# Kernel optimization log

Measured on AMD Instinct MI355X. Metric: run time of the kernel, lower is better.

## Reference

```python
import jax, jax.numpy as jnp
import numpy as np

N_NODES = 100000
N_EDGES = 3200000
F_IN = 54
H = 16


def gcn_conv(x, edge_index, W, b):
    """PyG GCNConv: linear -> add self-loops -> sym-normalized scatter-add -> +bias."""
    n = x.shape[0]
    x = x @ W  # [N, H] transform before propagation (PyG order)
    loop = jnp.arange(n, dtype=edge_index.dtype)
    src = jnp.concatenate([edge_index[0], loop])  # message sources
    dst = jnp.concatenate([edge_index[1], loop])  # aggregation targets
    deg = jax.ops.segment_sum(jnp.ones_like(dst, dtype=x.dtype), dst, num_segments=n)
    dinv = jnp.where(deg > 0, jax.lax.rsqrt(deg), 0.0)
    norm = dinv[src] * dinv[dst]  # D^-1/2 A_hat D^-1/2 edge weights
    msg = x[src] * norm[:, None]  # gather + scale, [E+N, H]
    out = jax.ops.segment_sum(msg, dst, num_segments=n)  # scatter-add
    return out + b


def setup_inputs() -> dict:
    key = jax.random.key(0)
    k = jax.random.split(key, 6)
    x = jax.random.normal(k[0], (N_NODES, F_IN), dtype=jnp.float32)
    edge_index = jax.random.randint(k[1], (2, N_EDGES), 0, N_NODES, dtype=jnp.int64)
    # Glorot-style init for GCNConv weights; bias zeros (PyG default)
    s1 = float(np.sqrt(6.0 / (F_IN + H)))
    s2 = float(np.sqrt(6.0 / (H + H)))
    W1 = jax.random.uniform(k[2], (F_IN, H), dtype=jnp.float32, minval=-s1, maxval=s1)
    b1 = jnp.zeros((H,), dtype=jnp.float32)
    W2 = jax.random.uniform(k[3], (H, H), dtype=jnp.float32, minval=-s2, maxval=s2)
    b2 = jnp.zeros((H,), dtype=jnp.float32)
    return {"x": x, "edge_index": edge_index, "W1": W1, "b1": b1, "W2": W2, "b2": b2}


def reference(x, edge_index, W1, b1, W2, b2):
    h = jax.nn.relu(gcn_conv(x, edge_index, W1, b1))
    # F.dropout(p=0.5, training=self.training) -> identity in eval mode
    h = jax.nn.relu(gcn_conv(h, edge_index, W2, b2))
    return h
```

## Files before the change

### kernel.cpp

```cpp
#include <hip/hip_runtime.h>
#include <hip/hip_fp16.h>

#define HDIM 16
#define FIN 54
#define BSHIFT 7
#define BNODES (1 << BSHIFT)
#define NBMAXB 800
#define NBBMAX 512
#define FBT 1024
#define LST 512
#define FPE 12544
#define PADCOL 6144
#define GTILE 256
#define GPAD 55

__global__ __launch_bounds__(FBT)
void fill_binned_kernel(const int* __restrict__ src, const int* __restrict__ dst,
                        int* __restrict__ lps, unsigned int* __restrict__ binned,
                        int E, int nb, int nbb, int per) {
    __shared__ unsigned int stage[FPE];
    __shared__ int lh[NBMAXB], lcur[NBMAXB];
    __shared__ int ls[FBT];
    int blk = blockIdx.x;
    int s0 = blk * per;
    int s1 = min(E, s0 + per);
    int tot = s1 - s0;
    int t = threadIdx.x;

    for (int b = t; b < nb; b += FBT) lh[b] = 0;
    __syncthreads();
    int idx = s0 + (t << 2);
    for (; idx + 3 < s1; idx += (FBT << 2)) {
        int4 d4 = *(const int4*)&dst[idx];
        atomicAdd(&lh[d4.x >> BSHIFT], 1);
        atomicAdd(&lh[d4.y >> BSHIFT], 1);
        atomicAdd(&lh[d4.z >> BSHIFT], 1);
        atomicAdd(&lh[d4.w >> BSHIFT], 1);
    }
    if (idx < s1) {
        int stop = min(idx + 4, s1);
        for (int e = idx; e < stop; ++e) atomicAdd(&lh[dst[e] >> BSHIFT], 1);
    }
    __syncthreads();
    ls[t] = (t < nb) ? lh[t] : 0;
    __syncthreads();
    for (int d = 1; d < FBT; d <<= 1) {
        int v = (t >= d) ? ls[t - d] : 0;
        __syncthreads();
        ls[t] += v;
        __syncthreads();
    }
    if (t <= nb) {
        int excl = ls[t] - ((t < nb) ? lh[t] : 0);
        if (t < nb) lcur[t] = excl;
        lps[t * nbb + blk] = excl;
    }
    __syncthreads();
    idx = s0 + (t << 2);
    for (; idx + 3 < s1; idx += (FBT << 2)) {
        int4 d4 = *(const int4*)&dst[idx];
        int4 v4 = *(const int4*)&src[idx];
        int p0 = atomicAdd(&lcur[d4.x >> BSHIFT], 1);
        int p1 = atomicAdd(&lcur[d4.y >> BSHIFT], 1);
        int p2 = atomicAdd(&lcur[d4.z >> BSHIFT], 1);
        int p3 = atomicAdd(&lcur[d4.w >> BSHIFT], 1);
        stage[p0] = ((unsigned int)v4.x << BSHIFT) | (unsigned int)(d4.x & (BNODES - 1));
        stage[p1] = ((unsigned int)v4.y << BSHIFT) | (unsigned int)(d4.y & (BNODES - 1));
        stage[p2] = ((unsigned int)v4.z << BSHIFT) | (unsigned int)(d4.z & (BNODES - 1));
        stage[p3] = ((unsigned int)v4.w << BSHIFT) | (unsigned int)(d4.w & (BNODES - 1));
    }
    if (idx < s1) {
        int stop = min(idx + 4, s1);
        for (int e = idx; e < stop; ++e) {
            int d = dst[e];
            int pos = atomicAdd(&lcur[d >> BSHIFT], 1);
            stage[pos] = ((unsigned int)src[e] << BSHIFT) | (unsigned int)(d & (BNODES - 1));
        }
    }
    __syncthreads();
    for (int k = t; k < tot; k += FBT) binned[s0 + k] = stage[k];
}

__global__ __launch_bounds__(LST)
void local_sort_kernel(const unsigned int* __restrict__ binned,
                       const int* __restrict__ lps,
                       unsigned int* __restrict__ col, int* __restrict__ cs,
                       int* __restrict__ ce, float* __restrict__ dinv,
                       int n, int nb, int nbb, int per) {
    __shared__ int st[NBBMAX], en[NBBMAX];
    __shared__ int hist[BNODES], scn[BNODES], cur[BNODES];
    int b = blockIdx.x;
    int t = threadIdx.x;
    int colbase = b * PADCOL;

    for (int blk = t; blk < nbb; blk += LST) {
        st[blk] = lps[b * nbb + blk];
        en[blk] = lps[(b + 1) * nbb + blk];
    }
    if (t < BNODES) hist[t] = 0;
    __syncthreads();

    int g = t >> 4, l = t & 15;
    for (int blk = g; blk < nbb; blk += (LST >> 4)) {
        int base = blk * per;
        int e = en[blk];
        for (int k = st[blk] + l; k < e; k += 16)
            atomicAdd(&hist[binned[base + k] & (BNODES - 1)], 1);
    }
    __syncthreads();
    if (t < BNODES) scn[t] = hist[t];
    __syncthreads();
    for (int d = 1; d < BNODES; d <<= 1) {
        int v = (t < BNODES && t >= d) ? scn[t - d] : 0;
        __syncthreads();
        if (t < BNODES) scn[t] += v;
        __syncthreads();
    }
    if (t < BNODES) {
        int excl = scn[t] - hist[t];
        cur[t] = excl;
        int node = (b << BSHIFT) + t;
        if (node < n) {
            cs[node] = colbase + excl;
            ce[node] = colbase + excl + hist[t];
            dinv[node] = rsqrtf((float)hist[t] + 1.0f);
        }
    }
    __syncthreads();
    for (int blk = g; blk < nbb; blk += (LST >> 4)) {
        int base = blk * per;
        int e = en[blk];
        for (int k = st[blk] + l; k < e; k += 16) {
            unsigned int p = binned[base + k];
            int pos = atomicAdd(&cur[p & (BNODES - 1)], 1);
            col[colbase + pos] = p >> BSHIFT;
        }
    }
}

__global__ __launch_bounds__(256)
void gemm_kernel(const float* __restrict__ X, const float* __restrict__ W,
                 const float* __restrict__ dinv, __half* __restrict__ Yh, int n) {
    __shared__ float Wl[FIN * HDIM];
    __shared__ float xl[GTILE * GPAD];
    for (int t = threadIdx.x; t < FIN * HDIM; t += blockDim.x) Wl[t] = W[t];

    int base = blockIdx.x * GTILE;
    int nrows = min(GTILE, n - base);
    const float* xb = X + (size_t)base * FIN;
    int tot = nrows * FIN;
    for (int i4 = threadIdx.x; i4 < (tot >> 2); i4 += blockDim.x) {
        float4 v = ((const float4*)xb)[i4];
        int i = i4 << 2;
        int r = i / FIN;
        int c = i - r * FIN;
#pragma unroll
        for (int u = 0; u < 4; ++u) {
            int cc = c + u, rr = r;
            if (cc >= FIN) { cc -= FIN; ++rr; }
            xl[rr * GPAD + cc] = (&v.x)[u];
        }
    }
    for (int i = (tot & ~3) + threadIdx.x; i < tot; i += blockDim.x) {
        int r = i / FIN;
        xl[r * GPAD + (i - r * FIN)] = xb[i];
    }
    __syncthreads();

    int t = threadIdx.x;
    if (t < nrows) {
        int row = base + t;
        const float* xr = &xl[t * GPAD];
        float acc[HDIM];
#pragma unroll
        for (int j = 0; j < HDIM; ++j) acc[j] = 0.0f;
#pragma unroll
        for (int k = 0; k < FIN; ++k) {
            float xv = xr[k];
#pragma unroll
            for (int j = 0; j < HDIM; ++j)
                acc[j] = fmaf(xv, Wl[k * HDIM + j], acc[j]);
        }
        float di = dinv[row];
        __half2 hh[8];
#pragma unroll
        for (int j = 0; j < 8; ++j)
            hh[j] = __floats2half2_rn(di * acc[2 * j], di * acc[2 * j + 1]);
        uint4* yo = (uint4*)(Yh + ((size_t)row << 4));
        yo[0] = *(uint4*)&hh[0];
        yo[1] = *(uint4*)&hh[4];
    }
}

__device__ __forceinline__ float4 ld_h4(const __half* __restrict__ hsh,
                                        unsigned int node, int q) {
    uint2 u = *(const uint2*)(hsh + ((size_t)node << 4) + (q << 2));
    __half2 a = *(__half2*)&u.x;
    __half2 b = *(__half2*)&u.y;
    float2 fa = __half22float2(a);
    float2 fb = __half22float2(b);
    return make_float4(fa.x, fa.y, fb.x, fb.y);
}

template <bool FUSE_W2>
__global__ void gather_kernel(const unsigned int* __restrict__ col,
                              const int* __restrict__ cs, const int* __restrict__ ce,
                              const __half* __restrict__ hsh, const float* __restrict__ dinv,
                              const float* __restrict__ bias, const float* __restrict__ W2,
                              __half* __restrict__ outh, float4* __restrict__ out4, int n) {
    __shared__ float4 W2l[HDIM * 4];
    if constexpr (FUSE_W2) {
        for (int t = threadIdx.x; t < HDIM * 4; t += blockDim.x)
            W2l[t] = ((const float4*)W2)[t];
        __syncthreads();
    }
    int idx = blockIdx.x * blockDim.x + threadIdx.x;
    int i = idx >> 3;
    int sub = idx & 7;
    int q = sub & 3;
    int h = sub >> 2;
    if (i >= n) return;
    int k0 = cs[i], k1 = ce[i];

    float4 acc = (h == 0) ? ld_h4(hsh, (unsigned int)i, q)
                          : make_float4(0.f, 0.f, 0.f, 0.f);
    int k = k0 + h;
    for (; k + 14 < k1; k += 16) {
        unsigned int s[8];
#pragma unroll
        for (int u = 0; u < 8; ++u) s[u] = col[k + 2 * u];
        float4 hv[8];
#pragma unroll
        for (int u = 0; u < 8; ++u) hv[u] = ld_h4(hsh, s[u], q);
#pragma unroll
        for (int u = 0; u < 8; ++u) {
            acc.x += hv[u].x; acc.y += hv[u].y; acc.z += hv[u].z; acc.w += hv[u].w;
        }
    }
    for (; k < k1; k += 2) {
        float4 hv = ld_h4(hsh, col[k], q);
        acc.x += hv.x; acc.y += hv.y; acc.z += hv.z; acc.w += hv.w;
    }
    acc.x += __shfl_xor(acc.x, 4);
    acc.y += __shfl_xor(acc.y, 4);
    acc.z += __shfl_xor(acc.z, 4);
    acc.w += __shfl_xor(acc.w, 4);

    float di = dinv[i];
    float4 b4 = ((const float4*)bias)[q];
    float4 r;
    r.x = fmaxf(fmaf(di, acc.x, b4.x), 0.0f);
    r.y = fmaxf(fmaf(di, acc.y, b4.y), 0.0f);
    r.z = fmaxf(fmaf(di, acc.z, b4.z), 0.0f);
    r.w = fmaxf(fmaf(di, acc.w, b4.w), 0.0f);

    if constexpr (FUSE_W2) {
        int lane = threadIdx.x & 63;
        int base = lane & ~7;
        float4 o = make_float4(0.f, 0.f, 0.f, 0.f);
#pragma unroll
        for (int p = 0; p < 4; ++p) {
            float rx = __shfl(r.x, base + p, 64);
            float ry = __shfl(r.y, base + p, 64);
            float rz = __shfl(r.z, base + p, 64);
            float rw = __shfl(r.w, base + p, 64);
            float4 w0 = W2l[(p * 4 + 0) * 4 + q];
            float4 w1 = W2l[(p * 4 + 1) * 4 + q];
            float4 w2 = W2l[(p * 4 + 2) * 4 + q];
            float4 w3 = W2l[(p * 4 + 3) * 4 + q];
            o.x = fmaf(rx, w0.x, fmaf(ry, w1.x, fmaf(rz, w2.x, fmaf(rw, w3.x, o.x))));
            o.y = fmaf(rx, w0.y, fmaf(ry, w1.y, fmaf(rz, w2.y, fmaf(rw, w3.y, o.y))));
            o.z = fmaf(rx, w0.z, fmaf(ry, w1.z, fmaf(rz, w2.z, fmaf(rw, w3.z, o.z))));
            o.w = fmaf(rx, w0.w, fmaf(ry, w1.w, fmaf(rz, w2.w, fmaf(rw, w3.w, o.w))));
        }
        if (h == 0) {
            __half2 o01 = __floats2half2_rn(di * o.x, di * o.y);
            __half2 o23 = __floats2half2_rn(di * o.z, di * o.w);
            uint2 pk;
            pk.x = *(unsigned int*)&o01;
            pk.y = *(unsigned int*)&o23;
            *(uint2*)(outh + ((size_t)i << 4) + (q << 2)) = pk;
        }
    } else {
        if (h == 0) out4[(size_t)i * 4 + q] = r;
    }
}

extern "C" void kernel_launch(void* const* d_in, const int* in_sizes, int n_in,
                              void* d_out, int out_size, void* d_ws, size_t ws_size,
                              hipStream_t stream) {
    const float* x  = (const float*)d_in[0];
    const int*   ei = (const int*)d_in[1];
    const float* W1 = (const float*)d_in[2];
    const float* b1 = (const float*)d_in[3];
    const float* W2 = (const float*)d_in[4];
    const float* b2 = (const float*)d_in[5];
    float* out = (float*)d_out;

    const int E = in_sizes[1] / 2;
    const int n = in_sizes[0] / FIN;
    const int* src = ei;
    const int* dst = ei + E;
    const int nb = (n + BNODES - 1) >> BSHIFT;

    int nbb = (E + 12499) / 12500;
    if (nbb > NBBMAX) nbb = NBBMAX;
    int per = (((E + nbb - 1) / nbb) + 3) & ~3;

    char* w = (char*)d_ws;
    auto take = [&](size_t bytes) { char* p = w; w += (bytes + 255) & ~(size_t)255; return p; };
    float* dinv = (float*)take((size_t)n * 4);
    int*   lps  = (int*)take((size_t)(nb + 1) * nbb * 4);
    int*   cs   = (int*)take((size_t)n * 4);
    int*   ce   = (int*)take((size_t)n * 4);
    size_t binned_sz = (size_t)nbb * per * 4;
    size_t h_sz      = (size_t)n * HDIM * 2 * 2;
    char*  X    = take(binned_sz > h_sz ? binned_sz : h_sz);
    unsigned int* binned = (unsigned int*)X;
    __half* hA  = (__half*)X;
    __half* hB  = (__half*)(X + (size_t)n * HDIM * 2);
    unsigned int* col = (unsigned int*)take((size_t)nb * PADCOL * 4);

    const int B = 256;

    fill_binned_kernel<<<nbb, FBT, 0, stream>>>(src, dst, lps, binned, E, nb, nbb, per);
    local_sort_kernel<<<nb, LST, 0, stream>>>(binned, lps, col, cs, ce, dinv, n, nb, nbb, per);

    gemm_kernel<<<(n + GTILE - 1) / GTILE, B, 0, stream>>>(x, W1, dinv, hA, n);

    gather_kernel<true><<<(n * 8 + B - 1) / B, B, 0, stream>>>(
        col, cs, ce, hA, dinv, b1, W2, hB, nullptr, n);

    gather_kernel<false><<<(n * 8 + B - 1) / B, B, 0, stream>>>(
        col, cs, ce, hB, dinv, b2, nullptr, nullptr, (float4*)out, n);
}
```

Baseline: 109.7 us.

## Fuse first-layer GEMM into the local sort kernel per node block

The separate X@W1 GEMM kernel is merged into the per-128-node local sort kernel. Each block loads its 128 rows of x and W1 into shared memory, computes the transformed features after the sort, and scales them by the degree normalisation it just computed in registers. This removes one kernel launch and the dinv reload. The cost is higher shared-memory use and only 128 of the 512 threads doing the GEMM. The binned and hA buffers no longer alias, since both are now live at the same time.

Result: faster. 102.3 us (-6.7%).

```diff
diff --git a/kernel.cpp b/kernel.cpp
--- a/kernel.cpp
+++ b/kernel.cpp
@@ -11,7 +11,6 @@
 #define LST 512
 #define FPE 12544
 #define PADCOL 6144
-#define GTILE 256
 #define GPAD 55
 
 __global__ __launch_bounds__(FBT)
@@ -82,16 +81,42 @@
 }
 
 __global__ __launch_bounds__(LST)
-void local_sort_kernel(const unsigned int* __restrict__ binned,
-                       const int* __restrict__ lps,
-                       unsigned int* __restrict__ col, int* __restrict__ cs,
-                       int* __restrict__ ce, float* __restrict__ dinv,
-                       int n, int nb, int nbb, int per) {
+void sort_gemm_kernel(const unsigned int* __restrict__ binned,
+                      const int* __restrict__ lps,
+                      const float* __restrict__ x, const float* __restrict__ W1,
+                      unsigned int* __restrict__ col, int* __restrict__ cs,
+                      int* __restrict__ ce, float* __restrict__ dinv,
+                      __half* __restrict__ hA,
+                      int n, int nb, int nbb, int per) {
     __shared__ int st[NBBMAX], en[NBBMAX];
     __shared__ int hist[BNODES], scn[BNODES], cur[BNODES];
+    __shared__ float Wl[FIN * HDIM];
+    __shared__ float xl[BNODES * GPAD];
     int b = blockIdx.x;
     int t = threadIdx.x;
     int colbase = b * PADCOL;
+    int row0 = b << BSHIFT;
+    int nrows = min(BNODES, n - row0);
+
+    const float* xb = x + (size_t)row0 * FIN;
+    int tot = nrows * FIN;
+    for (int i4 = t; i4 < (tot >> 2); i4 += LST) {
+        float4 v = ((const float4*)xb)[i4];
+        int i = i4 << 2;
+        int r = i / FIN;
+        int c = i - r * FIN;
+#pragma unroll
+        for (int u = 0; u < 4; ++u) {
+            int cc = c + u, rr = r;
+            if (cc >= FIN) { cc -= FIN; ++rr; }
+            xl[rr * GPAD + cc] = (&v.x)[u];
+        }
+    }
+    for (int i = (tot & ~3) + t; i < tot; i += LST) {
+        int r = i / FIN;
+        xl[r * GPAD + (i - r * FIN)] = xb[i];
+    }
+    for (int k = t; k < FIN * HDIM; k += LST) Wl[k] = W1[k];
 
     for (int blk = t; blk < nbb; blk += LST) {
         st[blk] = lps[b * nbb + blk];
@@ -116,14 +141,16 @@
         if (t < BNODES) scn[t] += v;
         __syncthreads();
     }
+    float di = 0.0f;
     if (t < BNODES) {
         int excl = scn[t] - hist[t];
         cur[t] = excl;
-        int node = (b << BSHIFT) + t;
+        int node = row0 + t;
+        di = rsqrtf((float)hist[t] + 1.0f);
         if (node < n) {
             cs[node] = colbase + excl;
             ce[node] = colbase + excl + hist[t];
-            dinv[node] = rsqrtf((float)hist[t] + 1.0f);
+            dinv[node] = di;
         }
     }
     __syncthreads();
@@ -136,40 +163,7 @@
             col[colbase + pos] = p >> BSHIFT;
         }
     }
-}
-
-__global__ __launch_bounds__(256)
-void gemm_kernel(const float* __restrict__ X, const float* __restrict__ W,
-                 const float* __restrict__ dinv, __half* __restrict__ Yh, int n) {
-    __shared__ float Wl[FIN * HDIM];
-    __shared__ float xl[GTILE * GPAD];
-    for (int t = threadIdx.x; t < FIN * HDIM; t += blockDim.x) Wl[t] = W[t];
-
-    int base = blockIdx.x * GTILE;
-    int nrows = min(GTILE, n - base);
-    const float* xb = X + (size_t)base * FIN;
-    int tot = nrows * FIN;
-    for (int i4 = threadIdx.x; i4 < (tot >> 2); i4 += blockDim.x) {
-        float4 v = ((const float4*)xb)[i4];
-        int i = i4 << 2;
-        int r = i / FIN;
-        int c = i - r * FIN;
-#pragma unroll
-        for (int u = 0; u < 4; ++u) {
-            int cc = c + u, rr = r;
-            if (cc >= FIN) { cc -= FIN; ++rr; }
-            xl[rr * GPAD + cc] = (&v.x)[u];
-        }
-    }
-    for (int i = (tot & ~3) + threadIdx.x; i < tot; i += blockDim.x) {
-        int r = i / FIN;
-        xl[r * GPAD + (i - r * FIN)] = xb[i];
-    }
-    __syncthreads();
-
-    int t = threadIdx.x;
     if (t < nrows) {
-        int row = base + t;
         const float* xr = &xl[t * GPAD];
         float acc[HDIM];
 #pragma unroll
@@ -181,12 +175,11 @@
             for (int j = 0; j < HDIM; ++j)
                 acc[j] = fmaf(xv, Wl[k * HDIM + j], acc[j]);
         }
-        float di = dinv[row];
         __half2 hh[8];
 #pragma unroll
         for (int j = 0; j < 8; ++j)
             hh[j] = __floats2half2_rn(di * acc[2 * j], di * acc[2 * j + 1]);
-        uint4* yo = (uint4*)(Yh + ((size_t)row << 4));
+        uint4* yo = (uint4*)(hA + ((size_t)(row0 + t) << 4));
         yo[0] = *(uint4*)&hh[0];
         yo[1] = *(uint4*)&hh[4];
     }
@@ -313,20 +306,16 @@
     int*   lps  = (int*)take((size_t)(nb + 1) * nbb * 4);
     int*   cs   = (int*)take((size_t)n * 4);
     int*   ce   = (int*)take((size_t)n * 4);
-    size_t binned_sz = (size_t)nbb * per * 4;
-    size_t h_sz      = (size_t)n * HDIM * 2 * 2;
-    char*  X    = take(binned_sz > h_sz ? binned_sz : h_sz);
-    unsigned int* binned = (unsigned int*)X;
-    __half* hA  = (__half*)X;
-    __half* hB  = (__half*)(X + (size_t)n * HDIM * 2);
+    unsigned int* binned = (unsigned int*)take((size_t)nbb * per * 4);
+    __half* hA  = (__half*)take((size_t)n * HDIM * 2);
+    __half* hB  = (__half*)take((size_t)n * HDIM * 2);
     unsigned int* col = (unsigned int*)take((size_t)nb * PADCOL * 4);
 
     const int B = 256;
 
     fill_binned_kernel<<<nbb, FBT, 0, stream>>>(src, dst, lps, binned, E, nb, nbb, per);
-    local_sort_kernel<<<nb, LST, 0, stream>>>(binned, lps, col, cs, ce, dinv, n, nb, nbb, per);
-
-    gemm_kernel<<<(n + GTILE - 1) / GTILE, B, 0, stream>>>(x, W1, dinv, hA, n);
+    sort_gemm_kernel<<<nb, LST, 0, stream>>>(binned, lps, x, W1, col, cs, ce, dinv,
+                                             hA, n, nb, nbb, per);
 
     gather_kernel<true><<<(n * 8 + B - 1) / B, B, 0, stream>>>(
         col, cs, ce, hA, dinv, b1, W2, hB, nullptr, n);
```
